# Optimization experiments

Measured on AMD Instinct MI355X. Metric: run time of the kernel, lower is better.

The kernel has to match this reference:

```python
import jax, jax.numpy as jnp
import numpy as np

N, IN_CAPS, IN_LEN = 32, 1152, 32
OUT_CAPS, OUT_LEN = 64, 32
NUM_ITERATIONS = 3


def setup_inputs() -> dict:
    key = jax.random.key(0)
    k1, k2 = jax.random.split(key)
    x = jax.random.normal(k1, (N, IN_CAPS, IN_LEN), dtype=jnp.float32)
    # learnable weight, torch.randn init: (out_capsules, out_length, in_length)
    weight = jax.random.normal(k2, (OUT_CAPS, OUT_LEN, IN_LEN), dtype=jnp.float32)
    return {"x": x, "weight": weight}


def _squash(v):
    # v * ||v|| / (1 + ||v||^2)  ==  (||v||^2/(1+||v||^2)) * v/||v||
    norm_sq = jnp.sum(v * v, axis=-1, keepdims=True)
    norm = jnp.sqrt(norm_sq)
    return v * norm / (1.0 + norm_sq)


def reference(x, weight):
    # priors u_hat: [N, out_caps, in_caps, out_len]
    priors = jnp.einsum('oli,bni->bonl', weight, x)
    logits = jnp.zeros_like(priors)
    output = None
    for r in range(NUM_ITERATIONS):
        # coupling coefficients: softmax over output capsules (axis=1)
        probs = jax.nn.softmax(logits, axis=1)
        # weighted sum over input capsules -> [N, out_caps, 1, out_len]
        output = jnp.sum(probs * priors, axis=-2, keepdims=True)
        if r != NUM_ITERATIONS - 1:
            output = _squash(output)
            # agreement update: [N, out_caps, in_caps, 1]
            logits = logits + jnp.sum(priors * output, axis=-1, keepdims=True)
    output = _squash(output)  # squash=True default
    return jnp.squeeze(output, axis=-2)  # [N, out_caps, out_len]
```

## Files before the change

### kernel.cpp

```cpp
#include <hip/hip_runtime.h>
#include <math.h>


#define N_B      32
#define IN_CAPS  1152
#define IN_LEN   32
#define OUT_CAPS 64
#define OUT_LEN  32

#define NCHUNK 16
#define NPB    (IN_CAPS / NCHUNK)
#define PASS_WAVES 4
#define NPW    (NPB / PASS_WAVES)
#define TSTR   36

#define DECODE_BC(d, b, c) \
    const int _slot = (d) >> 3; \
    const int b = ((d) & 7) * 4 + (_slot >> 4); \
    const int c = _slot & 15;

#define DPPV(v, ctrl) \
    __int_as_float(__builtin_amdgcn_update_dpp(0, __float_as_int(v), ctrl, 0xF, 0xF, true))

__device__ __forceinline__ float wave_max(float v) {
    v = fmaxf(v, DPPV(v, 0xB1));
    v = fmaxf(v, DPPV(v, 0x4E));
    v = fmaxf(v, DPPV(v, 0x141));
    v = fmaxf(v, DPPV(v, 0x140));
    v = fmaxf(v, __shfl_xor(v, 16, 64));
    v = fmaxf(v, __shfl_xor(v, 32, 64));
    return v;
}
__device__ __forceinline__ float wave_sum(float v) {
    v += DPPV(v, 0xB1);
    v += DPPV(v, 0x4E);
    v += DPPV(v, 0x141);
    v += DPPV(v, 0x140);
    v += __shfl_xor(v, 16, 64);
    v += __shfl_xor(v, 32, 64);
    return v;
}

__device__ __forceinline__ void pass_and_flush(const float* __restrict__ x,
                                               const float* T_row_src, int t_stride,
                                               float* buf,
                                               float* __restrict__ part_out,
                                               int b, int c, int tid, int lane, int wave) {
    float t[IN_LEN];
    {
#pragma unroll
        for (int q = 0; q < 8; ++q) {
            const float4 v = *(const float4*)&T_row_src[lane * t_stride + q * 4];
            t[4 * q] = v.x; t[4 * q + 1] = v.y; t[4 * q + 2] = v.z; t[4 * q + 3] = v.w;
        }
    }
    asm volatile("" : "+v"(t[0]), "+v"(t[1]), "+v"(t[2]), "+v"(t[3]),
                      "+v"(t[4]), "+v"(t[5]), "+v"(t[6]), "+v"(t[7]),
                      "+v"(t[8]), "+v"(t[9]), "+v"(t[10]), "+v"(t[11]),
                      "+v"(t[12]), "+v"(t[13]), "+v"(t[14]), "+v"(t[15]));
    asm volatile("" : "+v"(t[16]), "+v"(t[17]), "+v"(t[18]), "+v"(t[19]),
                      "+v"(t[20]), "+v"(t[21]), "+v"(t[22]), "+v"(t[23]),
                      "+v"(t[24]), "+v"(t[25]), "+v"(t[26]), "+v"(t[27]),
                      "+v"(t[28]), "+v"(t[29]), "+v"(t[30]), "+v"(t[31]));

    float s[IN_LEN];
#pragma unroll
    for (int i = 0; i < IN_LEN; ++i) s[i] = 0.f;

    const float* xw = x + ((size_t)b * IN_CAPS + c * NPB + wave * NPW) * IN_LEN;

#define L4(acc, R, k) \
    acc = fmaf((R).x, t[k],     acc); acc = fmaf((R).y, t[k + 1], acc); \
    acc = fmaf((R).z, t[k + 2], acc); acc = fmaf((R).w, t[k + 3], acc);
#define S4(R, k) \
    s[k]     = fmaf(prob, (R).x, s[k]);     s[k + 1] = fmaf(prob, (R).y, s[k + 1]); \
    s[k + 2] = fmaf(prob, (R).z, s[k + 2]); s[k + 3] = fmaf(prob, (R).w, s[k + 3]);

#pragma unroll
    for (int j = 0; j < NPW; ++j) {
        const float4* xr = (const float4*)(xw + j * IN_LEN);
        const float4 r0 = xr[0], r1 = xr[1], r2 = xr[2], r3 = xr[3],
                     r4 = xr[4], r5 = xr[5], r6 = xr[6], r7 = xr[7];

        float l0 = 0.f, l1 = 0.f, l2 = 0.f, l3 = 0.f;
        L4(l0, r0, 0)  L4(l1, r1, 4)  L4(l2, r2, 8)  L4(l3, r3, 12)
        L4(l0, r4, 16) L4(l1, r5, 20) L4(l2, r6, 24) L4(l3, r7, 28)
        const float logit = (l0 + l1) + (l2 + l3);

        const float m = wave_max(logit);
        const float p = __expf(logit - m);
        const float S = wave_sum(p);
        const float prob = p * __builtin_amdgcn_rcpf(S);

        S4(r0, 0)  S4(r1, 4)  S4(r2, 8)  S4(r3, 12)
        S4(r4, 16) S4(r5, 20) S4(r6, 24) S4(r7, 28)
    }
#undef L4
#undef S4

    {
        float4* dst = (float4*)&buf[(wave * OUT_CAPS + lane) * TSTR];
#pragma unroll
        for (int q = 0; q < 8; ++q)
            dst[q] = make_float4(s[4 * q], s[4 * q + 1], s[4 * q + 2], s[4 * q + 3]);
    }
    __syncthreads();
    {
        float4* pb4 = (float4*)(part_out + ((size_t)b * NCHUNK + c) * OUT_CAPS * IN_LEN);
        for (int e = tid; e < OUT_CAPS * IN_LEN / 4; e += 256) {
            const int o = e >> 3, q4 = (e & 7) * 4;
            const float4 a0 = *(const float4*)&buf[(0 * OUT_CAPS + o) * TSTR + q4];
            const float4 a1 = *(const float4*)&buf[(1 * OUT_CAPS + o) * TSTR + q4];
            const float4 a2 = *(const float4*)&buf[(2 * OUT_CAPS + o) * TSTR + q4];
            const float4 a3 = *(const float4*)&buf[(3 * OUT_CAPS + o) * TSTR + q4];
            pb4[e] = make_float4(a0.x + a1.x + a2.x + a3.x,
                                 a0.y + a1.y + a2.y + a3.y,
                                 a0.z + a1.z + a2.z + a3.z,
                                 a0.w + a1.w + a2.w + a3.w);
        }
    }
}

__global__ __launch_bounds__(256) void k_init(const float* __restrict__ x,
                                              const float* __restrict__ W,
                                              float* __restrict__ T) {
    const int b   = blockIdx.x;
    const int tid = threadIdx.x;
    const float* xb = x + (size_t)b * IN_CAPS * IN_LEN;

    __shared__ float4 red4[32][8];
    {
        const int q = tid & 7;
        const int g = tid >> 3;
        float4 acc = make_float4(0.f, 0.f, 0.f, 0.f);
        for (int n = g; n < IN_CAPS; n += 32) {
            const float4 v = *(const float4*)(xb + n * IN_LEN + q * 4);
            acc.x += v.x; acc.y += v.y; acc.z += v.z; acc.w += v.w;
        }
        red4[g][q] = acc;
    }
    __syncthreads();
    __shared__ float s0[IN_LEN];
    if (tid < 8) {
        float4 v = make_float4(0.f, 0.f, 0.f, 0.f);
        for (int g = 0; g < 32; ++g) {
            const float4 r = red4[g][tid];
            v.x += r.x; v.y += r.y; v.z += r.z; v.w += r.w;
        }
        const float inv = 1.f / 64.f;
        s0[tid * 4 + 0] = v.x * inv;
        s0[tid * 4 + 1] = v.y * inv;
        s0[tid * 4 + 2] = v.z * inv;
        s0[tid * 4 + 3] = v.w * inv;
    }
    __syncthreads();

    __shared__ float u[OUT_CAPS * OUT_LEN];
    for (int e = tid; e < OUT_CAPS * OUT_LEN; e += 256) {
        const float* wrow = W + (size_t)e * IN_LEN;
        float a = 0.f;
#pragma unroll
        for (int i = 0; i < IN_LEN; ++i) a = fmaf(wrow[i], s0[i], a);
        u[e] = a;
    }
    __syncthreads();

    __shared__ float scale[OUT_CAPS];
    if (tid < OUT_CAPS) {
        float ns = 0.f;
#pragma unroll
        for (int l = 0; l < OUT_LEN; ++l) { const float v = u[tid * OUT_LEN + l]; ns = fmaf(v, v, ns); }
        scale[tid] = sqrtf(ns) / (1.f + ns);
    }
    __syncthreads();

    for (int e = tid; e < OUT_CAPS * IN_LEN; e += 256) {
        const int o = e >> 5, i = e & 31;
        float a = 0.f;
#pragma unroll
        for (int l = 0; l < OUT_LEN; ++l)
            a = fmaf(W[((size_t)o * OUT_LEN + l) * IN_LEN + i], u[o * OUT_LEN + l], a);
        T[(size_t)b * OUT_CAPS * IN_LEN + e] = a * scale[o];
    }
}

__global__ __launch_bounds__(256, 2) void k_pass1(const float* __restrict__ x,
                                                  const float* __restrict__ T,
                                                  float* __restrict__ part) {
    DECODE_BC(blockIdx.x, b, c)
    const int tid  = threadIdx.x;
    const int lane = tid & 63;
    const int wave = __builtin_amdgcn_readfirstlane(tid >> 6);

    __shared__ __align__(16) float buf[PASS_WAVES * OUT_CAPS * TSTR];

    pass_and_flush(x, T + (size_t)b * OUT_CAPS * IN_LEN, IN_LEN,
                   buf, part, b, c, tid, lane, wave);
}

__global__ __launch_bounds__(256, 2) void kB(const float* __restrict__ x,
                                             const float* __restrict__ W,
                                             const float* __restrict__ T,
                                             const float* __restrict__ part,
                                             float* __restrict__ part2) {
    DECODE_BC(blockIdx.x, b, c)
    const int tid  = threadIdx.x;
    const int lane = tid & 63;
    const int wave = __builtin_amdgcn_readfirstlane(tid >> 6);

    __shared__ __align__(16) float T_lds[OUT_CAPS * TSTR];
    __shared__ __align__(16) float buf[PASS_WAVES * OUT_CAPS * TSTR];

    float* s_lds = buf;
    float* uu    = buf + 2048;
    float* sc    = buf + 4096;

    {
        const float4* pb4 = (const float4*)(part + (size_t)b * NCHUNK * OUT_CAPS * IN_LEN);
        for (int e = tid; e < OUT_CAPS * IN_LEN / 4; e += 256) {
            float4 acc = make_float4(0.f, 0.f, 0.f, 0.f);
#pragma unroll
            for (int cc = 0; cc < NCHUNK; ++cc) {
                const float4 v = pb4[cc * (OUT_CAPS * IN_LEN / 4) + e];
                acc.x += v.x; acc.y += v.y; acc.z += v.z; acc.w += v.w;
            }
            ((float4*)s_lds)[e] = acc;
        }
    }
    __syncthreads();
    for (int e = tid; e < OUT_CAPS * OUT_LEN; e += 256) {
        const int o = e >> 5;
        const float* wrow = W + (size_t)e * IN_LEN;
        const float* srow = s_lds + o * IN_LEN;
        float a = 0.f;
#pragma unroll
        for (int i = 0; i < IN_LEN; ++i) a = fmaf(wrow[i], srow[i], a);
        uu[e] = a;
    }
    __syncthreads();
    if (tid < OUT_CAPS) {
        float ns = 0.f;
#pragma unroll
        for (int l = 0; l < OUT_LEN; ++l) { const float v = uu[tid * OUT_LEN + l]; ns = fmaf(v, v, ns); }
        sc[tid] = sqrtf(ns) / (1.f + ns);
    }
    __syncthreads();

    for (int e = tid; e < OUT_CAPS * IN_LEN; e += 256) {
        const int o = e >> 5, i = e & 31;
        float a = 0.f;
#pragma unroll
        for (int l = 0; l < OUT_LEN; ++l)
            a = fmaf(W[((size_t)o * OUT_LEN + l) * IN_LEN + i], uu[o * OUT_LEN + l], a);
        T_lds[o * TSTR + i] = T[(size_t)b * OUT_CAPS * IN_LEN + e] + a * sc[o];
    }
    __syncthreads();

    pass_and_flush(x, T_lds, TSTR, buf, part2, b, c, tid, lane, wave);
}

__global__ __launch_bounds__(256) void kC(const float* __restrict__ W,
                                          const float* __restrict__ part2,
                                          float* __restrict__ out) {
    const int b   = blockIdx.x >> 3;
    const int og  = blockIdx.x & 7;
    const int tid = threadIdx.x;
    const int ol  = tid >> 5;
    const int i   = tid & 31;
    const int o   = og * 8 + ol;

    float a = 0.f;
    const float* pb = part2 + (size_t)b * NCHUNK * OUT_CAPS * IN_LEN + o * IN_LEN + i;
#pragma unroll
    for (int cc = 0; cc < NCHUNK; ++cc) a += pb[cc * OUT_CAPS * IN_LEN];

    __shared__ float s_lds[8][33];
    s_lds[ol][i] = a;
    __syncthreads();

    const float* wrow = W + ((size_t)o * OUT_LEN + i) * IN_LEN;
    float u = 0.f;
#pragma unroll
    for (int k = 0; k < IN_LEN; ++k) u = fmaf(wrow[k], s_lds[ol][k], u);

    float ns = u * u;
    ns += __shfl_xor(ns, 1, 64);
    ns += __shfl_xor(ns, 2, 64);
    ns += __shfl_xor(ns, 4, 64);
    ns += __shfl_xor(ns, 8, 64);
    ns += __shfl_xor(ns, 16, 64);
    const float scale = sqrtf(ns) / (1.f + ns);

    out[((size_t)b * OUT_CAPS + o) * OUT_LEN + i] = u * scale;
}

extern "C" void kernel_launch(void* const* d_in, const int* in_sizes, int n_in,
                              void* d_out, int out_size, void* d_ws, size_t ws_size,
                              hipStream_t stream) {
    const float* x = (const float*)d_in[0];
    const float* W = (const float*)d_in[1];
    float* out = (float*)d_out;

    float* T     = (float*)d_ws;
    float* part  = T + (size_t)N_B * OUT_CAPS * IN_LEN;
    float* part2 = part + (size_t)N_B * NCHUNK * OUT_CAPS * IN_LEN;

    k_init <<<N_B,          256, 0, stream>>>(x, W, T);
    k_pass1<<<N_B * NCHUNK, 256, 0, stream>>>(x, T, part);
    kB     <<<N_B * NCHUNK, 256, 0, stream>>>(x, W, T, part, part2);
    kC     <<<N_B * 8,      256, 0, stream>>>(W, part2, out);
}
```

Measured before the change: 130.0 us.

## Double chunk count and reduce waves via LDS atomics to raise occupancy

Splits input capsules into 32 chunks instead of 16, doubling the number of blocks per pass. The cross-wave reduction now uses LDS atomicAdd into a single padded buffer instead of a 4x staging buffer plus a summed readback. This shrinks shared memory so launch bounds can request 4 blocks per CU. The cost is more LDS atomic traffic, twice as many partials to write and reduce in kB and kC, and possible register pressure under the tighter bound.

```diff
diff --git a/kernel.cpp b/kernel.cpp
--- a/kernel.cpp
+++ b/kernel.cpp
@@ -8,16 +8,17 @@
 #define OUT_CAPS 64
 #define OUT_LEN  32
 
-#define NCHUNK 16
+#define NCHUNK 32
 #define NPB    (IN_CAPS / NCHUNK)
 #define PASS_WAVES 4
 #define NPW    (NPB / PASS_WAVES)
 #define TSTR   36
+#define SSTR   33
 
 #define DECODE_BC(d, b, c) \
     const int _slot = (d) >> 3; \
-    const int b = ((d) & 7) * 4 + (_slot >> 4); \
-    const int c = _slot & 15;
+    const int b = ((d) & 7) * 4 + (_slot >> 5); \
+    const int c = _slot & 31;
 
 #define DPPV(v, ctrl) \
     __int_as_float(__builtin_amdgcn_update_dpp(0, __float_as_int(v), ctrl, 0xF, 0xF, true))
@@ -41,11 +42,13 @@
     return v;
 }
 
-__device__ __forceinline__ void pass_and_flush(const float* __restrict__ x,
-                                               const float* T_row_src, int t_stride,
-                                               float* buf,
-                                               float* __restrict__ part_out,
-                                               int b, int c, int tid, int lane, int wave) {
+__device__ __forceinline__ void pass_atomic(const float* __restrict__ x,
+                                            const float* T_row_src, int t_stride,
+                                            float* s_red,
+                                            float* __restrict__ part_out,
+                                            int b, int c, int tid, int lane, int wave) {
+    for (int e = tid; e < OUT_CAPS * SSTR; e += 256) s_red[e] = 0.f;
+
     float t[IN_LEN];
     {
 #pragma unroll
@@ -98,26 +101,18 @@
 #undef L4
 #undef S4
 
-    {
-        float4* dst = (float4*)&buf[(wave * OUT_CAPS + lane) * TSTR];
-#pragma unroll
-        for (int q = 0; q < 8; ++q)
-            dst[q] = make_float4(s[4 * q], s[4 * q + 1], s[4 * q + 2], s[4 * q + 3]);
-    }
-    __syncthreads();
-    {
-        float4* pb4 = (float4*)(part_out + ((size_t)b * NCHUNK + c) * OUT_CAPS * IN_LEN);
-        for (int e = tid; e < OUT_CAPS * IN_LEN / 4; e += 256) {
-            const int o = e >> 3, q4 = (e & 7) * 4;
-            const float4 a0 = *(const float4*)&buf[(0 * OUT_CAPS + o) * TSTR + q4];
-            const float4 a1 = *(const float4*)&buf[(1 * OUT_CAPS + o) * TSTR + q4];
-            const float4 a2 = *(const float4*)&buf[(2 * OUT_CAPS + o) * TSTR + q4];
-            const float4 a3 = *(const float4*)&buf[(3 * OUT_CAPS + o) * TSTR + q4];
-            pb4[e] = make_float4(a0.x + a1.x + a2.x + a3.x,
-                                 a0.y + a1.y + a2.y + a3.y,
-                                 a0.z + a1.z + a2.z + a3.z,
-                                 a0.w + a1.w + a2.w + a3.w);
-        }
+    __syncthreads();
+    {
+        float* row = s_red + lane * SSTR;
+#pragma unroll
+        for (int i = 0; i < IN_LEN; ++i) atomicAdd(&row[i], s[i]);
+    }
+    __syncthreads();
+
+    {
+        float* pb = part_out + ((size_t)b * NCHUNK + c) * OUT_CAPS * IN_LEN;
+        for (int e = tid; e < OUT_CAPS * IN_LEN; e += 256)
+            pb[e] = s_red[(e >> 5) * SSTR + (e & 31)];
     }
 }
 
@@ -184,21 +179,22 @@
     }
 }
 
-__global__ __launch_bounds__(256, 2) void k_pass1(const float* __restrict__ x,
+__global__ __launch_bounds__(256, 4) void k_pass1(const float* __restrict__ x,
                                                   const float* __restrict__ T,
                                                   float* __restrict__ part) {
     DECODE_BC(blockIdx.x, b, c)
     const int tid  = threadIdx.x;
     const int lane = tid & 63;
     const int wave = __builtin_amdgcn_readfirstlane(tid >> 6);
-
-    __shared__ __align__(16) float buf[PASS_WAVES * OUT_CAPS * TSTR];
-
-    pass_and_flush(x, T + (size_t)b * OUT_CAPS * IN_LEN, IN_LEN,
-                   buf, part, b, c, tid, lane, wave);
-}
-
-__global__ __launch_bounds__(256, 2) void kB(const float* __restrict__ x,
+    (void)wave;
+
+    __shared__ __align__(16) float s_red[OUT_CAPS * SSTR];
+
+    pass_atomic(x, T + (size_t)b * OUT_CAPS * IN_LEN, IN_LEN,
+                s_red, part, b, c, tid, lane, wave);
+}
+
+__global__ __launch_bounds__(256, 4) void kB(const float* __restrict__ x,
                                              const float* __restrict__ W,
                                              const float* __restrict__ T,
                                              const float* __restrict__ part,
@@ -209,29 +205,28 @@
     const int wave = __builtin_amdgcn_readfirstlane(tid >> 6);
 
     __shared__ __align__(16) float T_lds[OUT_CAPS * TSTR];
-    __shared__ __align__(16) float buf[PASS_WAVES * OUT_CAPS * TSTR];
-
-    float* s_lds = buf;
-    float* uu    = buf + 2048;
-    float* sc    = buf + 4096;
+    __shared__ __align__(16) float s_red[OUT_CAPS * SSTR];
+    __shared__ __align__(16) float svt[OUT_CAPS * IN_LEN];
+    __shared__ __align__(16) float uu[OUT_CAPS * OUT_LEN];
+    __shared__ float sc[OUT_CAPS];
 
     {
         const float4* pb4 = (const float4*)(part + (size_t)b * NCHUNK * OUT_CAPS * IN_LEN);
         for (int e = tid; e < OUT_CAPS * IN_LEN / 4; e += 256) {
             float4 acc = make_float4(0.f, 0.f, 0.f, 0.f);
-#pragma unroll
+#pragma unroll 8
             for (int cc = 0; cc < NCHUNK; ++cc) {
                 const float4 v = pb4[cc * (OUT_CAPS * IN_LEN / 4) + e];
                 acc.x += v.x; acc.y += v.y; acc.z += v.z; acc.w += v.w;
             }
-            ((float4*)s_lds)[e] = acc;
+            ((float4*)svt)[e] = acc;
         }
     }
     __syncthreads();
     for (int e = tid; e < OUT_CAPS * OUT_LEN; e += 256) {
         const int o = e >> 5;
         const float* wrow = W + (size_t)e * IN_LEN;
-        const float* srow = s_lds + o * IN_LEN;
+        const float* srow = svt + o * IN_LEN;
         float a = 0.f;
 #pragma unroll
         for (int i = 0; i < IN_LEN; ++i) a = fmaf(wrow[i], srow[i], a);
@@ -256,7 +251,7 @@
     }
     __syncthreads();
 
-    pass_and_flush(x, T_lds, TSTR, buf, part2, b, c, tid, lane, wave);
+    pass_atomic(x, T_lds, TSTR, s_red, part2, b, c, tid, lane, wave);
 }
 
 __global__ __launch_bounds__(256) void kC(const float* __restrict__ W,
@@ -271,7 +266,7 @@
 
     float a = 0.f;
     const float* pb = part2 + (size_t)b * NCHUNK * OUT_CAPS * IN_LEN + o * IN_LEN + i;
-#pragma unroll
+#pragma unroll 8
     for (int cc = 0; cc < NCHUNK; ++cc) a += pb[cc * OUT_CAPS * IN_LEN];
 
     __shared__ float s_lds[8][33];
```

Measured after the change: 231.8 us. +78.3%, slower.
